# Kernel optimization log

Measured on AMD Instinct MI355X. Metric: run time of the kernel, lower is better.

Reference implementation:

```python
import jax, jax.numpy as jnp
import numpy as np

BG_CLASS = 3          # eval path drops argmax-class==3
NMS_THRESH = 0.2      # nms(rois, scores, 0.2)
IMG_SIZE = 512.0      # ClipBoxes to 512x512 image
NUM_CLASSES = 4


def _decode_boxes(rois, deltas):
    # BBoxTransform: std weights (0.1, 0.1, 0.2, 0.2), then clip to image
    w = rois[:, 2] - rois[:, 0]
    h = rois[:, 3] - rois[:, 1]
    cx = rois[:, 0] + 0.5 * w
    cy = rois[:, 1] + 0.5 * h
    dx = deltas[:, 0] * 0.1
    dy = deltas[:, 1] * 0.1
    dw = deltas[:, 2] * 0.2
    dh = deltas[:, 3] * 0.2
    pcx = cx + dx * w
    pcy = cy + dy * h
    pw = jnp.exp(dw) * w
    ph = jnp.exp(dh) * h
    boxes = jnp.stack([pcx - 0.5 * pw, pcy - 0.5 * ph,
                       pcx + 0.5 * pw, pcy + 0.5 * ph], axis=1)
    return jnp.clip(boxes, 0.0, IMG_SIZE)


def _iou_one_vs_all(box, boxes):
    x1 = jnp.maximum(box[0], boxes[:, 0])
    y1 = jnp.maximum(box[1], boxes[:, 1])
    x2 = jnp.minimum(box[2], boxes[:, 2])
    y2 = jnp.minimum(box[3], boxes[:, 3])
    inter = jnp.clip(x2 - x1, 0.0) * jnp.clip(y2 - y1, 0.0)
    area_a = (box[2] - box[0]) * (box[3] - box[1])
    area_b = (boxes[:, 2] - boxes[:, 0]) * (boxes[:, 3] - boxes[:, 1])
    return inter / (area_a + area_b - inter + 1e-8)


def _nms_keep_mask(boxes, scores, thresh):
    # Fixed-shape NMS: returns bool keep mask over the original ordering.
    N = boxes.shape[0]
    order = jnp.argsort(-scores)           # descending score
    b = boxes[order]
    idx = jnp.arange(N)

    def body(i, keep):
        iou = _iou_one_vs_all(b[i], b)
        suppress = (iou > thresh) & (idx > i)
        return jnp.where(keep[i], keep & ~suppress, keep)

    keep_sorted = jax.lax.fori_loop(0, N, body, jnp.ones((N,), dtype=bool))
    return jnp.zeros((N,), dtype=bool).at[order].set(keep_sorted)


def _head(f, rois, w6, b6, w7, b7, wc, bc, wr, br):
    # TwoMLPHead
    v = jax.nn.relu(f @ w6.T + b6)          # [N, 1024]
    v = jax.nn.relu(v @ w7.T + b7)          # [N, 1024]
    # FastRCNNPredictor
    c = v @ wc.T + bc                        # [N, num_classes]
    r = v @ wr.T + br                        # [N, num_classes*4]
    classes = jnp.argmax(c, axis=1)          # torch.max(x,1)[1]
    scores = jnp.max(c, axis=1)              # torch.max(x,1)[0]
    deltas = jnp.take_along_axis(r.reshape(-1, NUM_CLASSES, 4),
                                 classes[:, None, None], axis=1)[:, 0, :]
    boxes = _decode_boxes(rois, deltas)
    return scores, classes, boxes


def setup_inputs() -> dict:
    key = jax.random.key(0)
    ks = jax.random.split(key, 10)
    N, D, H = 8000, 12544, 1024
    f = jax.random.normal(ks[0], (N, D), dtype=jnp.float32)
    # valid xyxy ROIs inside 512x512
    xy = jax.random.uniform(ks[1], (N, 2), minval=0.0, maxval=380.0)
    wh = jax.random.uniform(ks[2], (N, 2), minval=20.0, maxval=120.0)
    rois = jnp.concatenate([xy, xy + wh], axis=1).astype(jnp.float32)
    w6 = jax.random.normal(ks[3], (H, D), dtype=jnp.float32) * 0.01
    b6 = jnp.zeros((H,), dtype=jnp.float32)
    w7 = jax.random.normal(ks[4], (H, H), dtype=jnp.float32) * 0.02
    b7 = jnp.zeros((H,), dtype=jnp.float32)
    wc = jax.random.normal(ks[5], (NUM_CLASSES, H), dtype=jnp.float32) * 0.02
    bc = jnp.zeros((NUM_CLASSES,), dtype=jnp.float32)
    wr = jax.random.normal(ks[6], (NUM_CLASSES * 4, H), dtype=jnp.float32) * 0.02
    br = jnp.zeros((NUM_CLASSES * 4,), dtype=jnp.float32)
    return {"f": f, "rois": rois, "w6": w6, "b6": b6, "w7": w7, "b7": b7,
            "wc": wc, "bc": bc, "wr": wr, "br": br}


def reference(f, rois, w6, b6, w7, b7, wc, bc, wr, br):
    scores, classes, boxes = _head(f, rois, w6, b6, w7, b7, wc, bc, wr, br)
    valid = classes != BG_CLASS
    s_masked = jnp.where(valid, scores, -jnp.inf)
    keep = _nms_keep_mask(boxes, s_masked, NMS_THRESH) & valid
    # fixed-shape equivalent of (scores[index], labels[index], bboxes[index])
    return scores, classes, boxes, keep
```

## Files before the change

kernel.cpp:

```cpp
#include <hip/hip_runtime.h>
#include <hip/hip_fp16.h>
#include <math.h>

typedef _Float16 f16;
typedef _Float16 f16x4 __attribute__((ext_vector_type(4)));
typedef _Float16 f16x8 __attribute__((ext_vector_type(8)));
typedef float f32x4 __attribute__((ext_vector_type(4)));
typedef unsigned long long u64;

#define GLD16(g, s) __builtin_amdgcn_global_load_lds( \
    (const __attribute__((address_space(1))) void*)(g), \
    (__attribute__((address_space(3))) void*)(s), 16, 0, 0)

struct HL { f16 h, l; };
__device__ __forceinline__ HL split1(float e) {
  float em = __uint_as_float(__float_as_uint(e) & 0xFFFFE000u);
  HL r;
  r.h = (f16)em;
  r.l = (f16)(e - em);
  return r;
}

__global__ __launch_bounds__(256) void split_kernel(const float* __restrict__ src,
                                                    f16* __restrict__ hi,
                                                    f16* __restrict__ lo,
                                                    long n4, float scale) {
  long stride = (long)gridDim.x * blockDim.x;
  for (long i = (long)blockIdx.x * blockDim.x + threadIdx.x; i < n4; i += stride) {
    float4 v = ((const float4*)src)[i];
    f16x4 h, l;
    HL r0 = split1(v.x * scale); h[0] = r0.h; l[0] = r0.l;
    HL r1 = split1(v.y * scale); h[1] = r1.h; l[1] = r1.l;
    HL r2 = split1(v.z * scale); h[2] = r2.h; l[2] = r2.l;
    HL r3 = split1(v.w * scale); h[3] = r3.h; l[3] = r3.l;
    ((f16x4*)hi)[i] = h;
    ((f16x4*)lo)[i] = l;
  }
}

__global__ __launch_bounds__(256) void gemm1_128(
    const float* __restrict__ Af,
    const f16* __restrict__ B1, const f16* __restrict__ B2,
    const float* __restrict__ bias,
    f16* __restrict__ out1, f16* __restrict__ out2,
    const int M, const int K) {
  __shared__ __align__(16) char smem[2][32768];
  const int tid = threadIdx.x;
  const int lane = tid & 63;
  const int wid = tid >> 6;
  const int wr = wid >> 1, wcol = wid & 1;
  const int m0 = blockIdx.y * 128;
  const int n0 = blockIdx.x * 128;

  f32x4 acc[4][4];
#pragma unroll
  for (int m = 0; m < 4; ++m)
#pragma unroll
    for (int n = 0; n < 4; ++n) acc[m][n] = (f32x4){0.f, 0.f, 0.f, 0.f};

  const float* gAf[4];
#pragma unroll
  for (int q = 0; q < 4; ++q) {
    int rowg = m0 + q * 32 + (tid >> 3);
    if (rowg > M - 1) rowg = M - 1;
    const int chunkg = (tid & 7) ^ ((tid >> 3) & 7);
    gAf[q] = Af + (size_t)rowg * K + chunkg * 4;
  }
  const int rq = tid >> 2;
  const int cg = (((tid & 3) ^ ((rq >> 1) & 3)) * 8);
  const f16* gB1q0 = B1 + (size_t)(n0 + rq) * K + cg;
  const f16* gB1q1 = B1 + (size_t)(n0 + 64 + rq) * K + cg;
  const f16* gB2q0 = B2 + (size_t)(n0 + rq) * K + cg;
  const f16* gB2q1 = B2 + (size_t)(n0 + 64 + rq) * K + cg;
  const int du = wid * 512;

  const int arow = wr * 64 + (lane & 15);
  const int brow = wcol * 64 + (lane & 15);
  const int kcB = (((lane >> 4) ^ ((brow >> 1) & 3)) * 8);
  const int pA0 = (((lane >> 4) * 2)     ^ (arow & 7)) * 4;
  const int pA1 = (((lane >> 4) * 2 + 1) ^ (arow & 7)) * 4;

  const int nt = K / 32;

#define STAGE(buf, kt)                                            \
  do {                                                            \
    char* smx_ = smem[buf];                                       \
    float* db = (float*)smx_;                                     \
    GLD16(gAf[0] + (kt), db + 0 * 1024 + wid * 256);              \
    GLD16(gAf[1] + (kt), db + 1 * 1024 + wid * 256);              \
    GLD16(gAf[2] + (kt), db + 2 * 1024 + wid * 256);              \
    GLD16(gAf[3] + (kt), db + 3 * 1024 + wid * 256);              \
    GLD16(gB1q0 + (kt), (f16*)(smx_ + 16384) + du);               \
    GLD16(gB1q1 + (kt), (f16*)(smx_ + 16384) + 2048 + du);        \
    GLD16(gB2q0 + (kt), (f16*)(smx_ + 24576) + du);               \
    GLD16(gB2q1 + (kt), (f16*)(smx_ + 24576) + 2048 + du);        \
  } while (0)

  STAGE(0, 0);

  for (int t = 0; t < nt; ++t) {
    asm volatile("s_waitcnt vmcnt(0)" ::: "memory");
    asm volatile("s_waitcnt lgkmcnt(0)" ::: "memory");
    __builtin_amdgcn_s_barrier();
    __builtin_amdgcn_sched_barrier(0);

    const char* smx = smem[t & 1];
    const float* sf = (const float*)smx;
    f16x8 a1[4], a2[4], b1[4], b2[4];
#pragma unroll
    for (int m = 0; m < 4; ++m) {
      const float* rp = sf + (arow + m * 16) * 32;
      f32x4 u = *(const f32x4*)(rp + pA0);
      f32x4 v = *(const f32x4*)(rp + pA1);
      f16x8 h, l;
#pragma unroll
      for (int j = 0; j < 4; ++j) { HL r = split1(u[j] * 256.0f); h[j] = r.h; l[j] = r.l; }
#pragma unroll
      for (int j = 0; j < 4; ++j) { HL r = split1(v[j] * 256.0f); h[4 + j] = r.h; l[4 + j] = r.l; }
      a1[m] = h; a2[m] = l;
    }
    {
      const f16* sb1 = (const f16*)(smx + 16384);
      const f16* sb2 = (const f16*)(smx + 24576);
#pragma unroll
      for (int n = 0; n < 4; ++n) {
        b1[n] = *(const f16x8*)&sb1[(brow + n * 16) * 32 + kcB];
        b2[n] = *(const f16x8*)&sb2[(brow + n * 16) * 32 + kcB];
      }
    }

    if (t + 1 < nt) STAGE((t + 1) & 1, (t + 1) * 32);

#pragma unroll
    for (int m = 0; m < 4; ++m)
#pragma unroll
      for (int n = 0; n < 4; ++n)
        acc[m][n] = __builtin_amdgcn_mfma_f32_16x16x32_f16(a1[m], b1[n], acc[m][n], 0, 0, 0);
#pragma unroll
    for (int m = 0; m < 4; ++m)
#pragma unroll
      for (int n = 0; n < 4; ++n)
        acc[m][n] = __builtin_amdgcn_mfma_f32_16x16x32_f16(a2[m], b1[n], acc[m][n], 0, 0, 0);
#pragma unroll
    for (int m = 0; m < 4; ++m)
#pragma unroll
      for (int n = 0; n < 4; ++n)
        acc[m][n] = __builtin_amdgcn_mfma_f32_16x16x32_f16(a1[m], b2[n], acc[m][n], 0, 0, 0);
  }
#undef STAGE

  const int crow = m0 + wr * 64 + 4 * (lane >> 4);
  const int ccol0 = n0 + wcol * 64 + (lane & 15);
#pragma unroll
  for (int n = 0; n < 4; ++n) {
    const int col = ccol0 + n * 16;
    const float bv = bias[col];
#pragma unroll
    for (int m = 0; m < 4; ++m) {
#pragma unroll
      for (int j = 0; j < 4; ++j) {
        const int row = crow + m * 16 + j;
        if (row < M) {
          float v = acc[m][n][j] * (1.0f / 65536.0f) + bv;
          v = fmaxf(v, 0.0f);
          HL r = split1(v * 256.0f);
          out1[(size_t)row * 1024 + col] = r.h;
          out2[(size_t)row * 1024 + col] = r.l;
        }
      }
    }
  }
}

__global__ __launch_bounds__(512) void gemm2_k(
    const f16* __restrict__ A1, const f16* __restrict__ A2,
    const f16* __restrict__ B1, const f16* __restrict__ B2,
    const float* __restrict__ bias,
    float* __restrict__ out1,
    const int M, const int K) {
  __shared__ __align__(16) char smem[3][49152];
  const int tid = threadIdx.x;
  const int lane = tid & 63;
  const int wid = tid >> 6;
  const int wr = wid >> 1, wcol = wid & 1;
  const int m0 = blockIdx.y * 256;
  const int n0 = blockIdx.x * 128;

  f32x4 acc[4][4];
#pragma unroll
  for (int m = 0; m < 4; ++m)
#pragma unroll
    for (int n = 0; n < 4; ++n) acc[m][n] = (f32x4){0.f, 0.f, 0.f, 0.f};

  const int cg = (((tid & 3) ^ ((tid >> 3) & 3)) * 8);
  const f16* gB1 = B1 + (size_t)(n0 + (tid >> 2)) * K + cg;
  const f16* gB2 = B2 + (size_t)(n0 + (tid >> 2)) * K + cg;
  int ra0 = m0 + (tid >> 2);       if (ra0 > M - 1) ra0 = M - 1;
  int ra1 = m0 + 128 + (tid >> 2); if (ra1 > M - 1) ra1 = M - 1;
  const f16* gA1q0 = A1 + (size_t)ra0 * K + cg;
  const f16* gA1q1 = A1 + (size_t)ra1 * K + cg;
  const f16* gA2q0 = A2 + (size_t)ra0 * K + cg;
  const f16* gA2q1 = A2 + (size_t)ra1 * K + cg;

  const int arow = wr * 64 + (lane & 15);
  const int brow = wcol * 64 + (lane & 15);
  const int kcA = (((lane >> 4) ^ ((arow >> 1) & 3)) * 8);
  const int kcB = (((lane >> 4) ^ ((brow >> 1) & 3)) * 8);

  const int nt = K / 32;

#define STAGE(buf, kt)                                            \
  do {                                                            \
    char* smx_ = smem[buf];                                       \
    f16* d1 = (f16*)smx_;                                         \
    f16* d2 = d1 + 8192;                                          \
    GLD16(gA1q0 + (kt), d1 + wid * 512);                          \
    GLD16(gA1q1 + (kt), d1 + 4096 + wid * 512);                   \
    GLD16(gA2q0 + (kt), d2 + wid * 512);                          \
    GLD16(gA2q1 + (kt), d2 + 4096 + wid * 512);                   \
    GLD16(gB1 + (kt), (f16*)(smx_ + 32768) + wid * 512);          \
    GLD16(gB2 + (kt), (f16*)(smx_ + 40960) + wid * 512);          \
  } while (0)

  STAGE(0, 0);
  if (nt > 1) STAGE(1, 32);
  int cur = 0;

  for (int t = 0; t < nt; ++t) {
    if (t + 1 < nt) asm volatile("s_waitcnt vmcnt(6)" ::: "memory");
    else            asm volatile("s_waitcnt vmcnt(0)" ::: "memory");
    asm volatile("s_waitcnt lgkmcnt(0)" ::: "memory");
    __builtin_amdgcn_s_barrier();
    __builtin_amdgcn_sched_barrier(0);

    const char* smx = smem[cur];
    const f16* s1 = (const f16*)smx;
    const f16* s2 = s1 + 8192;
    const f16* sb1 = (const f16*)(smx + 32768);
    const f16* sb2 = (const f16*)(smx + 40960);
    f16x8 a1[4], a2[4], b1[4], b2[4];
#pragma unroll
    for (int m = 0; m < 4; ++m) {
      a1[m] = *(const f16x8*)&s1[(arow + m * 16) * 32 + kcA];
      a2[m] = *(const f16x8*)&s2[(arow + m * 16) * 32 + kcA];
    }
#pragma unroll
    for (int n = 0; n < 4; ++n) {
      b1[n] = *(const f16x8*)&sb1[(brow + n * 16) * 32 + kcB];
      b2[n] = *(const f16x8*)&sb2[(brow + n * 16) * 32 + kcB];
    }

    int pre = cur + 2; if (pre >= 3) pre -= 3;
    if (t + 2 < nt) STAGE(pre, (t + 2) * 32);

#pragma unroll
    for (int m = 0; m < 4; ++m)
#pragma unroll
      for (int n = 0; n < 4; ++n)
        acc[m][n] = __builtin_amdgcn_mfma_f32_16x16x32_f16(a1[m], b1[n], acc[m][n], 0, 0, 0);
#pragma unroll
    for (int m = 0; m < 4; ++m)
#pragma unroll
      for (int n = 0; n < 4; ++n)
        acc[m][n] = __builtin_amdgcn_mfma_f32_16x16x32_f16(a2[m], b1[n], acc[m][n], 0, 0, 0);
#pragma unroll
    for (int m = 0; m < 4; ++m)
#pragma unroll
      for (int n = 0; n < 4; ++n)
        acc[m][n] = __builtin_amdgcn_mfma_f32_16x16x32_f16(a1[m], b2[n], acc[m][n], 0, 0, 0);

    ++cur; if (cur >= 3) cur = 0;
  }
#undef STAGE

  const int crow = m0 + wr * 64 + 4 * (lane >> 4);
  const int ccol0 = n0 + wcol * 64 + (lane & 15);
#pragma unroll
  for (int n = 0; n < 4; ++n) {
    const int col = ccol0 + n * 16;
    const float bv = bias[col];
#pragma unroll
    for (int m = 0; m < 4; ++m) {
#pragma unroll
      for (int j = 0; j < 4; ++j) {
        const int row = crow + m * 16 + j;
        if (row < M) {
          float v = acc[m][n][j] * (1.0f / 65536.0f) + bv;
          out1[(size_t)row * 1024 + col] = fmaxf(v, 0.0f);
        }
      }
    }
  }
}

__device__ __forceinline__ float dot4f(float4 a, float4 b) {
  return a.x * b.x + a.y * b.y + a.z * b.z + a.w * b.w;
}

__global__ __launch_bounds__(256) void head_final(
    const float* __restrict__ v7,
    const float* __restrict__ wc, const float* __restrict__ bc,
    const float* __restrict__ wr, const float* __restrict__ br,
    const float* __restrict__ rois,
    float* __restrict__ outScores, float* __restrict__ outClasses,
    float* __restrict__ outBoxes,
    float* __restrict__ smask, float* __restrict__ wsbox, int* __restrict__ wsval) {
  const int gw = (blockIdx.x * 256 + threadIdx.x) >> 6;
  const int lane = threadIdx.x & 63;
  if (gw >= 8000) return;

  const float4* vr = (const float4*)(v7 + (size_t)gw * 1024);
  float4 x0 = vr[lane], x1 = vr[64 + lane], x2 = vr[128 + lane], x3 = vr[192 + lane];

  float s[20];
#pragma unroll
  for (int o = 0; o < 20; ++o) {
    const float* wrow = (o < 4) ? (wc + o * 1024) : (wr + (o - 4) * 1024);
    const float4* w4 = (const float4*)wrow;
    float a = dot4f(x0, w4[lane]) + dot4f(x1, w4[64 + lane]) +
              dot4f(x2, w4[128 + lane]) + dot4f(x3, w4[192 + lane]);
#pragma unroll
    for (int off = 32; off >= 1; off >>= 1) a += __shfl_xor(a, off);
    s[o] = a + ((o < 4) ? bc[o] : br[o - 4]);
  }

  float best = s[0]; int cls = 0;
  if (s[1] > best) { best = s[1]; cls = 1; }
  if (s[2] > best) { best = s[2]; cls = 2; }
  if (s[3] > best) { best = s[3]; cls = 3; }

  float d0, d1, d2, d3;
  if      (cls == 0) { d0 = s[4];  d1 = s[5];  d2 = s[6];  d3 = s[7];  }
  else if (cls == 1) { d0 = s[8];  d1 = s[9];  d2 = s[10]; d3 = s[11]; }
  else if (cls == 2) { d0 = s[12]; d1 = s[13]; d2 = s[14]; d3 = s[15]; }
  else               { d0 = s[16]; d1 = s[17]; d2 = s[18]; d3 = s[19]; }

  float4 rb = ((const float4*)rois)[gw];
  float w = rb.z - rb.x, h = rb.w - rb.y;
  float cx = rb.x + 0.5f * w, cy = rb.y + 0.5f * h;
  float pcx = cx + d0 * 0.1f * w;
  float pcy = cy + d1 * 0.1f * h;
  float pw = expf(d2 * 0.2f) * w;
  float ph = expf(d3 * 0.2f) * h;
  float bx0 = fminf(fmaxf(pcx - 0.5f * pw, 0.f), 512.f);
  float by0 = fminf(fmaxf(pcy - 0.5f * ph, 0.f), 512.f);
  float bx1 = fminf(fmaxf(pcx + 0.5f * pw, 0.f), 512.f);
  float by1 = fminf(fmaxf(pcy + 0.5f * ph, 0.f), 512.f);

  if (lane == 0) {
    outScores[gw] = best;
    outClasses[gw] = (float)cls;
    outBoxes[gw * 4 + 0] = bx0;
    outBoxes[gw * 4 + 1] = by0;
    outBoxes[gw * 4 + 2] = bx1;
    outBoxes[gw * 4 + 3] = by1;
    int valid = (cls != 3);
    smask[gw] = valid ? best : -INFINITY;
    wsval[gw] = valid;
    float4 bb; bb.x = bx0; bb.y = by0; bb.z = bx1; bb.w = by1;
    ((float4*)wsbox)[gw] = bb;
  }
}

__global__ __launch_bounds__(256) void rank_kernel(
    const float* __restrict__ smask, const float* __restrict__ bx,
    const int* __restrict__ valid,
    int* __restrict__ order, float* __restrict__ sboxes, int* __restrict__ svalid) {
  __shared__ __align__(16) float sS[8000];
  const int tid = threadIdx.x;
  for (int i = tid; i < 8000; i += 256) sS[i] = smask[i];
  __syncthreads();
  const int i = blockIdx.x * 256 + tid;
  if (i >= 8000) return;
  const float si = sS[i];
  int cnt = 0;
  const float4* s4p = (const float4*)sS;
  for (int j4 = 0; j4 < 2000; j4 += 4) {
    float4 sa = s4p[j4], sb = s4p[j4 + 1], sc = s4p[j4 + 2], sd = s4p[j4 + 3];
    int jb = j4 * 4;
    cnt += (sa.x > si) || (sa.x == si && (jb + 0) < i);
    cnt += (sa.y > si) || (sa.y == si && (jb + 1) < i);
    cnt += (sa.z > si) || (sa.z == si && (jb + 2) < i);
    cnt += (sa.w > si) || (sa.w == si && (jb + 3) < i);
    cnt += (sb.x > si) || (sb.x == si && (jb + 4) < i);
    cnt += (sb.y > si) || (sb.y == si && (jb + 5) < i);
    cnt += (sb.z > si) || (sb.z == si && (jb + 6) < i);
    cnt += (sb.w > si) || (sb.w == si && (jb + 7) < i);
    cnt += (sc.x > si) || (sc.x == si && (jb + 8) < i);
    cnt += (sc.y > si) || (sc.y == si && (jb + 9) < i);
    cnt += (sc.z > si) || (sc.z == si && (jb + 10) < i);
    cnt += (sc.w > si) || (sc.w == si && (jb + 11) < i);
    cnt += (sd.x > si) || (sd.x == si && (jb + 12) < i);
    cnt += (sd.y > si) || (sd.y == si && (jb + 13) < i);
    cnt += (sd.z > si) || (sd.z == si && (jb + 14) < i);
    cnt += (sd.w > si) || (sd.w == si && (jb + 15) < i);
  }
  order[cnt] = i;
  svalid[cnt] = valid[i];
  ((float4*)sboxes)[cnt] = ((const float4*)bx)[i];
}

__global__ __launch_bounds__(256) void iou_matrix(const float* __restrict__ sboxes,
                                                  u64* __restrict__ MT,
                                                  u64* __restrict__ Mdiag,
                                                  const int* __restrict__ svalid) {
  const int t = blockIdx.y;
  const int w = blockIdx.x * 4 + (threadIdx.x >> 6);
  if (w < t || w >= 125) return;
  if (svalid[t * 64] == 0 || svalid[w * 64] == 0) return;
  const int lane = threadIdx.x & 63;
  const int ri = t * 64 + lane;
  float4 rb = ((const float4*)sboxes)[ri];
  const float ra = (rb.z - rb.x) * (rb.w - rb.y);
  const float4* cb = (const float4*)sboxes + w * 64;
  u64 bits = 0;
#pragma unroll 4
  for (int j = 0; j < 64; ++j) {
    float4 c = cb[j];
    float x1 = fmaxf(rb.x, c.x), y1 = fmaxf(rb.y, c.y);
    float x2 = fminf(rb.z, c.z), y2 = fminf(rb.w, c.w);
    float inter = fmaxf(x2 - x1, 0.f) * fmaxf(y2 - y1, 0.f);
    float ca = (c.z - c.x) * (c.w - c.y);
    float iou = inter / (ra + ca - inter + 1e-8f);
    int gc = w * 64 + j;
    if (iou > 0.2f && gc > ri) bits |= (1ULL << j);
  }
  MT[((size_t)t * 125 + w) * 64 + lane] = bits;
  if (w == t) Mdiag[(size_t)t * 64 + lane] = bits;
}

__global__ __launch_bounds__(128) void nms_scan(
    const u64* __restrict__ MT, const u64* __restrict__ Mdiag,
    const int* __restrict__ order,
    const int* __restrict__ svalid, float* __restrict__ outKeep) {
  __shared__ __align__(16) u64 sMdiag[8000];
  __shared__ u64 acc[126];
  __shared__ unsigned char klist[64];
  __shared__ int kcount;
  __shared__ int tv[125];
  __shared__ int nvt_s;
  const int tid = threadIdx.x;
  for (int i = tid; i < 4000; i += 128)
    ((float4*)sMdiag)[i] = ((const float4*)Mdiag)[i];
  for (int w = tid; w < 125; w += 128) acc[w] = 0;
  if (tid < 125) tv[tid] = svalid[tid * 64];
  __syncthreads();
  if (tid == 0) {
    int c = 0;
    while (c < 125 && tv[c]) ++c;
    nvt_s = c;
  }
  __syncthreads();
  const int nvt = nvt_s;

  for (int t = 0; t < nvt; ++t) {
    if (tid < 64) {
      u64 myrow = sMdiag[t * 64 + tid];
      unsigned mlo = (unsigned)myrow, mhi = (unsigned)(myrow >> 32);
      u64 r = acc[t];
      u64 rem = ~r;
      while (rem) {
        int i = __builtin_ctzll(rem);
        unsigned rlo = (unsigned)__builtin_amdgcn_readlane((int)mlo, i);
        unsigned rhi = (unsigned)__builtin_amdgcn_readlane((int)mhi, i);
        u64 rowi = ((u64)rhi << 32) | (u64)rlo;
        r |= rowi;
        rem &= ~(rowi | (1ULL << i));
      }
      u64 kept = ~r;
      if (tid == 0) { acc[t] = r; kcount = (int)__popcll(kept); }
      if ((kept >> tid) & 1ULL)
        klist[__popcll(kept & ((1ULL << tid) - 1ULL))] = (unsigned char)tid;
    }
    __syncthreads();
    const int kc = kcount;
    const int w = t + 1 + tid;
    if (w < nvt) {
      u64 a = acc[w];
      const u64* base = MT + ((size_t)t * 125 + w) * 64;
      int j = 0;
      for (; j + 16 <= kc; j += 16) {
        u64 o = 0;
#pragma unroll
        for (int q = 0; q < 16; ++q) o |= base[klist[j + q]];
        a |= o;
      }
      for (; j + 4 <= kc; j += 4) {
        u64 v0 = base[klist[j]];
        u64 v1 = base[klist[j + 1]];
        u64 v2 = base[klist[j + 2]];
        u64 v3 = base[klist[j + 3]];
        a |= (v0 | v1) | (v2 | v3);
      }
      for (; j < kc; ++j) a |= base[klist[j]];
      acc[w] = a;
    }
    __syncthreads();
  }

  for (int p = tid; p < 8000; p += 128) {
    int removed = (int)((acc[p >> 6] >> (p & 63)) & 1ULL);
    float kv = (!removed && svalid[p]) ? 1.0f : 0.0f;
    outKeep[order[p]] = kv;
  }
}

extern "C" void kernel_launch(void* const* d_in, const int* in_sizes, int n_in,
                              void* d_out, int out_size, void* d_ws, size_t ws_size,
                              hipStream_t stream) {
  const float* F    = (const float*)d_in[0];
  const float* ROIS = (const float*)d_in[1];
  const float* W6   = (const float*)d_in[2];
  const float* B6   = (const float*)d_in[3];
  const float* W7   = (const float*)d_in[4];
  const float* B7   = (const float*)d_in[5];
  const float* WC   = (const float*)d_in[6];
  const float* BC   = (const float*)d_in[7];
  const float* WR   = (const float*)d_in[8];
  const float* BR   = (const float*)d_in[9];

  const size_t N = 8000, D = 12544, H = 1024;
  char* ws = (char*)d_ws;
  size_t off = 0;
  auto alloc = [&](size_t bytes) -> void* {
    void* p = (void*)(ws + off);
    off += (bytes + 255) & ~(size_t)255;
    return p;
  };
  f16*   B1w   = (f16*)alloc(H * D * 2);
  f16*   B2w   = (f16*)alloc(H * D * 2);
  f16*   V61   = (f16*)alloc(N * H * 2);
  f16*   V62   = (f16*)alloc(N * H * 2);
  f16*   W71   = (f16*)alloc(H * H * 2);
  f16*   W72   = (f16*)alloc(H * H * 2);
  float* V7    = (float*)alloc(N * H * 4);
  float* SMASK = (float*)alloc(N * 4);
  float* WSBOX = (float*)alloc(N * 16);
  int*   WSVAL = (int*)alloc(N * 4);
  int*   ORDER = (int*)alloc(N * 4);
  float* SBOX  = (float*)alloc(N * 16);
  int*   SVAL  = (int*)alloc(N * 4);
  u64*   MT    = (u64*)alloc((size_t)125 * 125 * 64 * 8);
  u64*   MDIAG = (u64*)alloc(125 * 64 * 8);

  float* outScores  = (float*)d_out;
  float* outClasses = (float*)d_out + 8000;
  float* outBoxes   = (float*)d_out + 16000;
  float* outKeep    = (float*)d_out + 48000;

  split_kernel<<<1024, 256, 0, stream>>>(W6, B1w, B2w, (long)(H * D / 4), 256.0f);
  split_kernel<<<256, 256, 0, stream>>>(W7, W71, W72, (long)(H * H / 4), 256.0f);

  gemm1_128<<<dim3(8, 63), 256, 0, stream>>>(F, B1w, B2w, B6, V61, V62, 8000, 12544);
  gemm2_k<<<dim3(8, 32), 512, 0, stream>>>(V61, V62, W71, W72, B7, V7, 8000, 1024);

  head_final<<<2000, 256, 0, stream>>>(V7, WC, BC, WR, BR, ROIS,
                                       outScores, outClasses, outBoxes,
                                       SMASK, WSBOX, WSVAL);
  rank_kernel<<<32, 256, 0, stream>>>(SMASK, WSBOX, WSVAL, ORDER, SBOX, SVAL);
  iou_matrix<<<dim3(32, 125), 256, 0, stream>>>(SBOX, MT, MDIAG, SVAL);
  nms_scan<<<1, 128, 0, stream>>>(MT, MDIAG, ORDER, SVAL, outKeep);
}
```

Before: 1.168 ms.

## Use packed f16 conversion in GEMM split and row-major IoU mask layout

The GEMM A-operand hi/lo split now converts pairs of floats with the packed round-toward-zero convert instead of eight scalar conversions, which cuts VALU work in the inner loop. Because the hi part has its low mantissa bits masked off, truncating it is exact, while the lo part may now round differently. The IoU suppression mask moves from a per-tile transposed layout to row-major [box][128 words]. In the NMS scan, each thread reads one column word per kept row with a 1 KB stride, so neighbouring threads hit adjacent addresses.

```diff
diff --git a/kernel.cpp b/kernel.cpp
--- a/kernel.cpp
+++ b/kernel.cpp
@@ -3,6 +3,7 @@
 #include <math.h>
 
 typedef _Float16 f16;
+typedef _Float16 f16x2 __attribute__((ext_vector_type(2)));
 typedef _Float16 f16x4 __attribute__((ext_vector_type(4)));
 typedef _Float16 f16x8 __attribute__((ext_vector_type(8)));
 typedef float f32x4 __attribute__((ext_vector_type(4)));
@@ -19,6 +20,32 @@
   r.h = (f16)em;
   r.l = (f16)(e - em);
   return r;
+}
+
+__device__ __forceinline__ void splitcvt8(f32x4 u, f32x4 v, f16x8& H, f16x8& L) {
+  union { f16x2 h2[4]; f16x8 h8; } uh, ul;
+#pragma unroll
+  for (int p = 0; p < 2; ++p) {
+    float a = u[2 * p] * 256.0f, b = u[2 * p + 1] * 256.0f;
+    float am = __uint_as_float(__float_as_uint(a) & 0xFFFFE000u);
+    float bm = __uint_as_float(__float_as_uint(b) & 0xFFFFE000u);
+    auto pk = __builtin_amdgcn_cvt_pkrtz(am, bm);
+    uh.h2[p] = *reinterpret_cast<f16x2*>(&pk);
+    auto pl = __builtin_amdgcn_cvt_pkrtz(a - am, b - bm);
+    ul.h2[p] = *reinterpret_cast<f16x2*>(&pl);
+  }
+#pragma unroll
+  for (int p = 0; p < 2; ++p) {
+    float a = v[2 * p] * 256.0f, b = v[2 * p + 1] * 256.0f;
+    float am = __uint_as_float(__float_as_uint(a) & 0xFFFFE000u);
+    float bm = __uint_as_float(__float_as_uint(b) & 0xFFFFE000u);
+    auto pk = __builtin_amdgcn_cvt_pkrtz(am, bm);
+    uh.h2[2 + p] = *reinterpret_cast<f16x2*>(&pk);
+    auto pl = __builtin_amdgcn_cvt_pkrtz(a - am, b - bm);
+    ul.h2[2 + p] = *reinterpret_cast<f16x2*>(&pl);
+  }
+  H = uh.h8;
+  L = ul.h8;
 }
 
 __global__ __launch_bounds__(256) void split_kernel(const float* __restrict__ src,
@@ -112,12 +139,7 @@
       const float* rp = sf + (arow + m * 16) * 32;
       f32x4 u = *(const f32x4*)(rp + pA0);
       f32x4 v = *(const f32x4*)(rp + pA1);
-      f16x8 h, l;
-#pragma unroll
-      for (int j = 0; j < 4; ++j) { HL r = split1(u[j] * 256.0f); h[j] = r.h; l[j] = r.l; }
-#pragma unroll
-      for (int j = 0; j < 4; ++j) { HL r = split1(v[j] * 256.0f); h[4 + j] = r.h; l[4 + j] = r.l; }
-      a1[m] = h; a2[m] = l;
+      splitcvt8(u, v, a1[m], a2[m]);
     }
     {
       const f16* sb1 = (const f16*)(smx + 16384);
@@ -401,7 +423,7 @@
 }
 
 __global__ __launch_bounds__(256) void iou_matrix(const float* __restrict__ sboxes,
-                                                  u64* __restrict__ MT,
+                                                  u64* __restrict__ M,
                                                   u64* __restrict__ Mdiag,
                                                   const int* __restrict__ svalid) {
   const int t = blockIdx.y;
@@ -425,12 +447,12 @@
     int gc = w * 64 + j;
     if (iou > 0.2f && gc > ri) bits |= (1ULL << j);
   }
-  MT[((size_t)t * 125 + w) * 64 + lane] = bits;
+  M[(size_t)ri * 128 + w] = bits;
   if (w == t) Mdiag[(size_t)t * 64 + lane] = bits;
 }
 
 __global__ __launch_bounds__(128) void nms_scan(
-    const u64* __restrict__ MT, const u64* __restrict__ Mdiag,
+    const u64* __restrict__ M, const u64* __restrict__ Mdiag,
     const int* __restrict__ order,
     const int* __restrict__ svalid, float* __restrict__ outKeep) {
   __shared__ __align__(16) u64 sMdiag[8000];
@@ -477,22 +499,22 @@
     const int w = t + 1 + tid;
     if (w < nvt) {
       u64 a = acc[w];
-      const u64* base = MT + ((size_t)t * 125 + w) * 64;
+      const u64* base = M + (size_t)t * 64 * 128 + w;
       int j = 0;
       for (; j + 16 <= kc; j += 16) {
         u64 o = 0;
 #pragma unroll
-        for (int q = 0; q < 16; ++q) o |= base[klist[j + q]];
+        for (int q = 0; q < 16; ++q) o |= base[(size_t)klist[j + q] * 128];
         a |= o;
       }
       for (; j + 4 <= kc; j += 4) {
-        u64 v0 = base[klist[j]];
-        u64 v1 = base[klist[j + 1]];
-        u64 v2 = base[klist[j + 2]];
-        u64 v3 = base[klist[j + 3]];
+        u64 v0 = base[(size_t)klist[j] * 128];
+        u64 v1 = base[(size_t)klist[j + 1] * 128];
+        u64 v2 = base[(size_t)klist[j + 2] * 128];
+        u64 v3 = base[(size_t)klist[j + 3] * 128];
         a |= (v0 | v1) | (v2 | v3);
       }
-      for (; j < kc; ++j) a |= base[klist[j]];
+      for (; j < kc; ++j) a |= base[(size_t)klist[j] * 128];
       acc[w] = a;
     }
     __syncthreads();
@@ -540,7 +562,7 @@
   int*   ORDER = (int*)alloc(N * 4);
   float* SBOX  = (float*)alloc(N * 16);
   int*   SVAL  = (int*)alloc(N * 4);
-  u64*   MT    = (u64*)alloc((size_t)125 * 125 * 64 * 8);
+  u64*   MM    = (u64*)alloc(N * 128 * 8);
   u64*   MDIAG = (u64*)alloc(125 * 64 * 8);
 
   float* outScores  = (float*)d_out;
@@ -558,6 +580,6 @@
                                        outScores, outClasses, outBoxes,
                                        SMASK, WSBOX, WSVAL);
   rank_kernel<<<32, 256, 0, stream>>>(SMASK, WSBOX, WSVAL, ORDER, SBOX, SVAL);
-  iou_matrix<<<dim3(32, 125), 256, 0, stream>>>(SBOX, MT, MDIAG, SVAL);
-  nms_scan<<<1, 128, 0, stream>>>(MT, MDIAG, ORDER, SVAL, outKeep);
-}
+  iou_matrix<<<dim3(32, 125), 256, 0, stream>>>(SBOX, MM, MDIAG, SVAL);
+  nms_scan<<<1, 128, 0, stream>>>(MM, MDIAG, ORDER, SVAL, outKeep);
+}
```

After: 1.153 ms. About the same (-1.3%).
